# Kernel tuning notes

Hardware: AMD Instinct MI355X
Metric: run time of the kernel (lower is better)

The kernel has to match this reference:

```python
import math
import jax, jax.numpy as jnp
import numpy as np

N_EMBD = 1024
N_HEAD = 16
NUM_BUCKETS = 32
MAX_DISTANCE = 128


def _relative_position_bucket(relative_position, num_buckets=NUM_BUCKETS, max_distance=MAX_DISTANCE):
    # unidirectional (bidirectional=False): rp = -min(rp, 0)
    rp = -jnp.minimum(relative_position, 0)
    max_exact = num_buckets // 2
    is_small = rp < max_exact
    rp_large = max_exact + (
        jnp.log(rp.astype(jnp.float32) / max_exact + 1e-10)
        / math.log(max_distance / max_exact)
        * (num_buckets - max_exact)
    ).astype(jnp.int32)
    rp_large = jnp.minimum(rp_large, num_buckets - 1)
    return jnp.where(is_small, rp, rp_large)


def setup_inputs() -> dict:
    key = jax.random.key(0)
    ks = jax.random.split(key, 6)
    B, T, C = 4, 2048, N_EMBD
    s_in = 1.0 / math.sqrt(C)
    x = jax.random.normal(ks[0], (B, T, C), dtype=jnp.float32)
    W_attn = jax.random.normal(ks[1], (3 * C, C), dtype=jnp.float32) * s_in
    b_attn = jnp.zeros((3 * C,), dtype=jnp.float32)
    W_proj = jax.random.normal(ks[2], (C, C), dtype=jnp.float32) * s_in
    b_proj = jnp.zeros((C,), dtype=jnp.float32)
    rel_emb = jax.random.normal(ks[3], (NUM_BUCKETS, N_HEAD), dtype=jnp.float32) * 0.02
    return {"x": x, "W_attn": W_attn, "b_attn": b_attn,
            "W_proj": W_proj, "b_proj": b_proj, "rel_emb": rel_emb}


def reference(x, W_attn, b_attn, W_proj, b_proj, rel_emb):
    B, T, C = x.shape
    H = N_HEAD
    D = C // H
    qkv = x @ W_attn.T + b_attn              # [B,T,3C]
    q, k, v = jnp.split(qkv, 3, axis=-1)
    q = q.reshape(B, T, H, D).transpose(0, 2, 1, 3)  # [B,H,T,D]
    k = k.reshape(B, T, H, D).transpose(0, 2, 1, 3)
    v = v.reshape(B, T, H, D).transpose(0, 2, 1, 3)

    # T5 relative position bias (unidirectional)
    pos = jnp.arange(T)
    rel_pos = pos[None, :] - pos[:, None]            # [T,T] key - query
    buckets = _relative_position_bucket(rel_pos)     # [T,T]
    rel_bias = rel_emb[buckets]                      # [T,T,H]
    rel_bias = rel_bias.transpose(2, 0, 1)[None]     # [1,H,T,T]

    att = jnp.einsum('bhqd,bhkd->bhqk', q, k) * (1.0 / math.sqrt(D))
    att = att + rel_bias
    causal = jnp.tril(jnp.ones((T, T), dtype=bool))
    att = jnp.where(causal[None, None], att, -jnp.inf)
    att = jax.nn.softmax(att, axis=-1)
    y = jnp.einsum('bhqk,bhkd->bhqd', att, v)        # [B,H,T,D]
    y = y.transpose(0, 2, 1, 3).reshape(B, T, C)
    y = y @ W_proj.T + b_proj
    return y
```

## Files before the change

### kernel.cpp

```cpp
#include <hip/hip_runtime.h>
#include <hip/hip_bf16.h>

typedef __attribute__((ext_vector_type(8))) short short8;
typedef __attribute__((ext_vector_type(4))) short short4v;
typedef __attribute__((ext_vector_type(4))) float f32x4;

#define DEVI static __device__ __forceinline__

#define MTOK 8192
#define CDIM 1024
#define HN 16
#define HD 64
#define TSEQ 2048

#if defined(__has_builtin)
#if __has_builtin(__builtin_amdgcn_exp2f)
#define EXP2(x) __builtin_amdgcn_exp2f(x)
#else
#define EXP2(x) exp2f(x)
#endif
#else
#define EXP2(x) exp2f(x)
#endif

DEVI short bf16_rne(float f) {
  union { float f; unsigned u; } v; v.f = f;
  unsigned r = v.u + 0x7FFFu + ((v.u >> 16) & 1u);
  return (short)(r >> 16);
}

DEVI unsigned cvt_pk_bf16(float lo, float hi) {
  unsigned r;
  asm("v_cvt_pk_bf16_f32 %0, %1, %2" : "=v"(r) : "v"(lo), "v"(hi));
  return r;
}

DEVI void gload16(const void* g, void* l) {
  __builtin_amdgcn_global_load_lds(
      (const __attribute__((address_space(1))) void*)(unsigned long long)g,
      (__attribute__((address_space(3))) void*)(unsigned long long)l, 16, 0, 0);
}

#define MFMA_B16(A,B,C) __builtin_amdgcn_mfma_f32_16x16x32_bf16(A,B,C,0,0,0)

__global__ void pack_kernel(const float* __restrict__ x, const float* __restrict__ Wa,
                            const float* __restrict__ Wp,
                            short* __restrict__ xb, short* __restrict__ wab,
                            short* __restrict__ wpb) {
  const int NX4 = MTOK*CDIM/4, NA4 = 3*CDIM*CDIM/4, NP4 = CDIM*CDIM/4;
  const int total = NX4 + NA4 + NP4;
  for (int i = blockIdx.x*blockDim.x + threadIdx.x; i < total; i += gridDim.x*blockDim.x) {
    const float* src; short* dst; int off;
    if (i < NX4)          { src = x;  dst = xb;  off = i*4; }
    else if (i < NX4+NA4) { src = Wa; dst = wab; off = (i-NX4)*4; }
    else                  { src = Wp; dst = wpb; off = (i-NX4-NA4)*4; }
    float4 v = *(const float4*)(src + off);
    short4v r;
    r.x = bf16_rne(v.x); r.y = bf16_rne(v.y); r.z = bf16_rne(v.z); r.w = bf16_rne(v.w);
    *(short4v*)(dst + off) = r;
  }
}

__global__ void bias_table_kernel(const float* __restrict__ rel_emb, float* __restrict__ tab) {
  int d = blockIdx.x*blockDim.x + threadIdx.x;
  if (d >= TSEQ) return;
  int bucket;
  if (d < 16) bucket = d;
  else {
    int bl = 16 + (int)(logf((float)d / 16.0f + 1e-10f) / 2.0794415416798357f * 16.0f);
    bucket = bl < 31 ? bl : 31;
  }
  for (int h = 0; h < HN; h++) tab[h*TSEQ + d] = rel_emb[bucket*HN + h];
}

template<int EPI>
__global__ __launch_bounds__(512)
void gemm2(const short* __restrict__ A, const short* __restrict__ B,
           const float* __restrict__ bias,
           short* __restrict__ oq, short* __restrict__ ok, short* __restrict__ vt,
           float* __restrict__ of) {
  const int K = CDIM;
  int nbx = gridDim.x;
  int idx = blockIdx.y * nbx + blockIdx.x;
  int cpx = (nbx * gridDim.y) >> 3;
  int sw = (idx & 7) * cpx + (idx >> 3);
  int n0 = (sw % nbx) * 128, m0 = (sw / nbx) * 256;

  int tid = threadIdx.x, lane = tid & 63, w = tid >> 6;
  int wm = w >> 1, wn = w & 1;
  int r16 = lane & 15, g = lane >> 4;

  __shared__ __align__(16) short As[3][256*32];
  __shared__ __align__(16) short Bs[3][128*32];

  f32x4 zf = {0.f,0.f,0.f,0.f};
  f32x4 acc[4][4];
  #pragma unroll
  for (int mf = 0; mf < 4; mf++)
    #pragma unroll
    for (int nf = 0; nf < 4; nf++) acc[mf][nf] = zf;

  int r0 = tid >> 2;
  int cswz = (((tid & 3) ^ ((r0 >> 1) & 3)) << 3);
  long long aofs = (long long)(m0 + r0) * K + cswz;
  long long bofs = (long long)(n0 + r0) * K + cswz;

  auto STAGE = [&](int kt, int bi) {
    gload16(A + aofs + kt*32,          (short*)As[bi] + tid*8);
    gload16(A + aofs + kt*32 + 128*K,  (short*)As[bi] + 4096 + tid*8);
    gload16(B + bofs + kt*32,          (short*)Bs[bi] + tid*8);
  };

  STAGE(0, 0); STAGE(1, 1);
  asm volatile("s_waitcnt vmcnt(3)" ::: "memory");
  __builtin_amdgcn_s_barrier();
  __builtin_amdgcn_sched_barrier(0);

  int swz3 = (r16 >> 1) & 3;
  int fbA = (wm*64 + r16)*32 + ((g ^ swz3) << 3);
  int fbB = (wn*64 + r16)*32 + ((g ^ swz3) << 3);

  for (int kt = 0; kt < 32; kt++) {
    int cur = kt % 3;
    if (kt < 30) STAGE(kt + 2, (kt + 2) % 3);
    const short* Ab = As[cur];
    const short* Bb = Bs[cur];
    short8 af[4], bf[4];
    #pragma unroll
    for (int mf = 0; mf < 4; mf++) af[mf] = *(const short8*)(Ab + fbA + mf*512);
    #pragma unroll
    for (int nf = 0; nf < 4; nf++) bf[nf] = *(const short8*)(Bb + fbB + nf*512);
    __builtin_amdgcn_s_setprio(1);
    #pragma unroll
    for (int mf = 0; mf < 4; mf++)
      #pragma unroll
      for (int nf = 0; nf < 4; nf++)
        acc[mf][nf] = MFMA_B16(af[mf], bf[nf], acc[mf][nf]);
    __builtin_amdgcn_s_setprio(0);
    if (kt < 30) asm volatile("s_waitcnt vmcnt(3)" ::: "memory");
    else         asm volatile("s_waitcnt vmcnt(0)" ::: "memory");
    __builtin_amdgcn_s_barrier();
    __builtin_amdgcn_sched_barrier(0);
  }

  int b = m0 >> 11;
  int mrel = (m0 & 2047) + wm*64 + g*4;
  if constexpr (EPI == 0) {
    int which = n0 >> 10;
    int hh = ((n0 & 1023) >> 6) + wn;
    long long bh = (long long)(b*HN + hh);
    #pragma unroll
    for (int nf = 0; nf < 4; nf++) {
      int dd = nf*16 + r16;
      float bv = bias[n0 + wn*64 + dd];
      if (which == 2) {
        short* vdst = vt + (bh*HD + dd)*TSEQ + mrel;
        #pragma unroll
        for (int mf = 0; mf < 4; mf++) {
          short4v pv;
          #pragma unroll
          for (int j = 0; j < 4; j++) pv[j] = bf16_rne(acc[mf][nf][j] + bv);
          *(short4v*)(vdst + mf*16) = pv;
        }
      } else {
        short* odst = (which == 0 ? oq : ok) + bh*TSEQ*HD + dd;
        #pragma unroll
        for (int mf = 0; mf < 4; mf++)
          #pragma unroll
          for (int j = 0; j < 4; j++)
            odst[(long long)(mrel + mf*16 + j)*HD] = bf16_rne(acc[mf][nf][j] + bv);
      }
    }
  } else {
    #pragma unroll
    for (int nf = 0; nf < 4; nf++) {
      int col = n0 + wn*64 + nf*16 + r16;
      float bv = bias[col];
      #pragma unroll
      for (int mf = 0; mf < 4; mf++)
        #pragma unroll
        for (int j = 0; j < 4; j++)
          of[(long long)(m0 + wm*64 + mf*16 + g*4 + j)*CDIM + col] = acc[mf][nf][j] + bv;
    }
  }
}

__global__ __launch_bounds__(256)
void attn_kernel(const short* __restrict__ Qg, const short* __restrict__ Kg,
                 const short* __restrict__ Vtg, const float* __restrict__ btab,
                 short* __restrict__ outp) {
  int bh = blockIdx.x;
  int qb = 15 - (int)blockIdx.y;
  int h = bh & (HN-1), b = bh >> 4;
  int q0 = qb * 128;
  int tid = threadIdx.x, lane = tid & 63, w = tid >> 6;
  int r16 = lane & 15, g = lane >> 4;

  __shared__ __align__(16) short Ks[64*64];
  __shared__ __align__(16) short Vs[64*64];
  __shared__ __align__(16) short Ps[8][1024];
  __shared__ float bias_s[256];

  bias_s[tid & 255] = btab[h*TSEQ + (tid & 255)] * 1.44269504f;
  float cb = btab[h*TSEQ + 255] * 1.44269504f;

  short8 qa[2][2];
  #pragma unroll
  for (int mi = 0; mi < 2; mi++)
    #pragma unroll
    for (int ks = 0; ks < 2; ks++)
      qa[mi][ks] = *(const short8*)(Qg + ((long long)bh*TSEQ + q0 + w*32 + mi*16 + r16)*HD + ks*32 + g*8);

  f32x4 zf = {0.f,0.f,0.f,0.f};
  f32x4 o[2][4];
  #pragma unroll
  for (int mi = 0; mi < 2; mi++)
    #pragma unroll
    for (int c = 0; c < 4; c++) o[mi][c] = zf;
  float m_[2] = {-1e30f, -1e30f}, l_[2] = {0.f, 0.f};

  const short8 ones = {0x3f80,0x3f80,0x3f80,0x3f80,0x3f80,0x3f80,0x3f80,0x3f80};
  int qmax_wave = q0 + w*32 + 31;
  int swz = r16 & 7;
  int qrel = q0 + w*32 + r16;
  const float SC = 0.18033688f;

  for (int kb = 0; kb < q0 + 128; kb += 64) {
    #pragma unroll
    for (int i = 0; i < 2; i++) {
      int idx = tid + i*256;
      int r = idx >> 3;
      int cq = ((idx & 7) ^ (r & 7)) * 8;
      gload16(Kg  + ((long long)bh*TSEQ + kb + r)*HD + cq, (short*)Ks + idx*8);
      gload16(Vtg + ((long long)bh*HD  + r)*TSEQ + kb + cq, (short*)Vs + idx*8);
    }
    __syncthreads();
    if (kb <= qmax_wave) {
      f32x4 s[2][4];
      #pragma unroll
      for (int mi = 0; mi < 2; mi++)
        #pragma unroll
        for (int n = 0; n < 4; n++) s[mi][n] = zf;
      #pragma unroll
      for (int n = 0; n < 4; n++) {
        #pragma unroll
        for (int ks = 0; ks < 2; ks++) {
          short8 kf = *(const short8*)&Ks[(n*16 + r16)*64 + ((ks*4 + g) ^ swz)*8];
          s[0][n] = MFMA_B16(kf, qa[0][ks], s[0][n]);
          s[1][n] = MFMA_B16(kf, qa[1][ks], s[1][n]);
        }
      }
      bool far = (kb + 176 <= q0 + w*32);
      #pragma unroll
      for (int mi = 0; mi < 2; mi++) {
        char* prow = (char*)Ps[w*2 + mi] + r16*128 + ((g & 1) << 3);
        if (far) {
          float smax = s[mi][0][0];
          #pragma unroll
          for (int n = 0; n < 4; n++)
            #pragma unroll
            for (int j = 0; j < 4; j++) smax = fmaxf(smax, s[mi][n][j]);
          float mx = smax*SC + cb;
          mx = fmaxf(mx, __shfl_xor(mx, 16));
          mx = fmaxf(mx, __shfl_xor(mx, 32));
          float mnew;
          if (__all(mx <= m_[mi] + 8.0f)) {
            mnew = m_[mi];
          } else {
            mnew = fmaxf(m_[mi], mx);
            float corr = EXP2(m_[mi] - mnew);
            l_[mi] *= corr;
            #pragma unroll
            for (int c = 0; c < 4; c++) o[mi][c] *= corr;
            m_[mi] = mnew;
          }
          float cc = cb - mnew;
          #pragma unroll
          for (int n = 0; n < 4; n++) {
            unsigned u0 = cvt_pk_bf16(EXP2(__builtin_fmaf(s[mi][n][0], SC, cc)),
                                      EXP2(__builtin_fmaf(s[mi][n][1], SC, cc)));
            unsigned u1 = cvt_pk_bf16(EXP2(__builtin_fmaf(s[mi][n][2], SC, cc)),
                                      EXP2(__builtin_fmaf(s[mi][n][3], SC, cc)));
            *(uint2*)(prow + ((((n*2 + (g >> 1)) ^ swz)) << 4)) = make_uint2(u0, u1);
          }
        } else {
          int dbase = qrel + mi*16 - kb - g*4;
          float rowv[4][4];
          #pragma unroll
          for (int n = 0; n < 4; n++)
            #pragma unroll
            for (int j = 0; j < 4; j++) {
              int d = dbase - n*16 - j;
              rowv[n][j] = (d >= 0) ? s[mi][n][j]*SC + bias_s[d] : -1e30f;
            }
          float mx = rowv[0][0];
          #pragma unroll
          for (int n = 0; n < 4; n++)
            #pragma unroll
            for (int j = 0; j < 4; j++) mx = fmaxf(mx, rowv[n][j]);
          mx = fmaxf(mx, __shfl_xor(mx, 16));
          mx = fmaxf(mx, __shfl_xor(mx, 32));
          float mnew;
          if (__all(mx <= m_[mi] + 8.0f)) {
            mnew = m_[mi];
          } else {
            mnew = fmaxf(m_[mi], mx);
            float corr = EXP2(m_[mi] - mnew);
            l_[mi] *= corr;
            #pragma unroll
            for (int c = 0; c < 4; c++) o[mi][c] *= corr;
            m_[mi] = mnew;
          }
          #pragma unroll
          for (int n = 0; n < 4; n++) {
            unsigned u0 = cvt_pk_bf16(EXP2(rowv[n][0] - mnew), EXP2(rowv[n][1] - mnew));
            unsigned u1 = cvt_pk_bf16(EXP2(rowv[n][2] - mnew), EXP2(rowv[n][3] - mnew));
            *(uint2*)(prow + ((((n*2 + (g >> 1)) ^ swz)) << 4)) = make_uint2(u0, u1);
          }
        }
      }
      f32x4 lacc[2] = {zf, zf};
      #pragma unroll
      for (int ks = 0; ks < 2; ks++) {
        short8 pf0 = *(const short8*)((char*)Ps[w*2+0] + r16*128 + (((ks*4 + g) ^ swz) << 4));
        short8 pf1 = *(const short8*)((char*)Ps[w*2+1] + r16*128 + (((ks*4 + g) ^ swz) << 4));
        lacc[0] = MFMA_B16(ones, pf0, lacc[0]);
        lacc[1] = MFMA_B16(ones, pf1, lacc[1]);
        #pragma unroll
        for (int c = 0; c < 4; c++) {
          short8 vf = *(const short8*)&Vs[(c*16 + r16)*64 + ((ks*4 + g) ^ swz)*8];
          o[0][c] = MFMA_B16(vf, pf0, o[0][c]);
          o[1][c] = MFMA_B16(vf, pf1, o[1][c]);
        }
      }
      l_[0] += lacc[0][0];
      l_[1] += lacc[1][0];
    }
    __syncthreads();
  }

  #pragma unroll
  for (int mi = 0; mi < 2; mi++) {
    float inv = 1.0f / l_[mi];
    long long base = ((long long)(b*TSEQ + qrel + mi*16))*CDIM + h*HD;
    #pragma unroll
    for (int c = 0; c < 4; c++) {
      #pragma unroll
      for (int jj = 0; jj < 2; jj++) {
        unsigned pv = cvt_pk_bf16(o[mi][c][jj*2]*inv, o[mi][c][jj*2+1]*inv);
        *(unsigned*)(outp + base + c*16 + g*4 + jj*2) = pv;
      }
    }
  }
}

extern "C" void kernel_launch(void* const* d_in, const int* in_sizes, int n_in,
                              void* d_out, int out_size, void* d_ws, size_t ws_size,
                              hipStream_t stream) {
  (void)in_sizes; (void)n_in; (void)out_size; (void)ws_size;
  const float* x      = (const float*)d_in[0];
  const float* W_attn = (const float*)d_in[1];
  const float* b_attn = (const float*)d_in[2];
  const float* W_proj = (const float*)d_in[3];
  const float* b_proj = (const float*)d_in[4];
  const float* rel    = (const float*)d_in[5];
  float* out = (float*)d_out;
  char* ws = (char*)d_ws;

  short* xb   = (short*)(ws);
  short* wab  = (short*)(ws + 16777216LL);
  short* wpb  = (short*)(ws + 23068672LL);
  short* qbuf = (short*)(ws + 25165824LL);
  short* kbuf = (short*)(ws + 41943040LL);
  short* vt   = (short*)(ws + 58720256LL);
  short* att  = (short*)(ws + 75497472LL);
  float* tab  = (float*)(ws + 92274688LL);

  pack_kernel<<<2048, 256, 0, stream>>>(x, W_attn, W_proj, xb, wab, wpb);
  bias_table_kernel<<<8, 256, 0, stream>>>(rel, tab);
  gemm2<0><<<dim3(24, 32), 512, 0, stream>>>(xb, wab, b_attn, qbuf, kbuf, vt, nullptr);
  attn_kernel<<<dim3(64, 16), 256, 0, stream>>>(qbuf, kbuf, vt, tab, att);
  gemm2<1><<<dim3(8, 32), 512, 0, stream>>>(att, wpb, b_proj, nullptr, nullptr, nullptr, out);
}
```

Measured before the change: 249.7 us.

## Double-buffer K/V tiles in attention kernel with async global-to-LDS prefetch

Splits the K and V shared-memory tiles into two buffers and prefetches the tile two steps ahead, so global loads overlap the MFMA work on the current tile. The plain __syncthreads pairs are replaced by explicit vmcnt waits and raw barriers. This doubles K/V LDS use, which can lower occupancy. It also relies on the gload16 direct-to-LDS loads being counted by vmcnt, and if that counting assumption is wrong the results are incorrect.

Result: slower. 255.1 us (+2.2%).

```diff
diff --git a/kernel.cpp b/kernel.cpp
--- a/kernel.cpp
+++ b/kernel.cpp
@@ -196,13 +196,25 @@
   int tid = threadIdx.x, lane = tid & 63, w = tid >> 6;
   int r16 = lane & 15, g = lane >> 4;
 
-  __shared__ __align__(16) short Ks[64*64];
-  __shared__ __align__(16) short Vs[64*64];
+  __shared__ __align__(16) short Ks[2][64*64];
+  __shared__ __align__(16) short Vs[2][64*64];
   __shared__ __align__(16) short Ps[8][1024];
   __shared__ float bias_s[256];
 
   bias_s[tid & 255] = btab[h*TSEQ + (tid & 255)] * 1.44269504f;
   float cb = btab[h*TSEQ + 255] * 1.44269504f;
+
+  auto STAGE = [&](int t, int bi) {
+    int kb = t * 64;
+    #pragma unroll
+    for (int i = 0; i < 2; i++) {
+      int idx = tid + i*256;
+      int r = idx >> 3;
+      int cq = ((idx & 7) ^ (r & 7)) * 8;
+      gload16(Kg  + ((long long)bh*TSEQ + kb + r)*HD + cq, (short*)Ks[bi] + idx*8);
+      gload16(Vtg + ((long long)bh*HD  + r)*TSEQ + kb + cq, (short*)Vs[bi] + idx*8);
+    }
+  };
 
   short8 qa[2][2];
   #pragma unroll
@@ -224,17 +236,20 @@
   int swz = r16 & 7;
   int qrel = q0 + w*32 + r16;
   const float SC = 0.18033688f;
-
-  for (int kb = 0; kb < q0 + 128; kb += 64) {
-    #pragma unroll
-    for (int i = 0; i < 2; i++) {
-      int idx = tid + i*256;
-      int r = idx >> 3;
-      int cq = ((idx & 7) ^ (r & 7)) * 8;
-      gload16(Kg  + ((long long)bh*TSEQ + kb + r)*HD + cq, (short*)Ks + idx*8);
-      gload16(Vtg + ((long long)bh*HD  + r)*TSEQ + kb + cq, (short*)Vs + idx*8);
-    }
-    __syncthreads();
+  int ntiles = (q0 + 128) >> 6;
+
+  STAGE(0, 0);
+  STAGE(1, 1);
+  asm volatile("s_waitcnt lgkmcnt(0)" ::: "memory");
+
+  for (int t = 0; t < ntiles; t++) {
+    if (t + 1 < ntiles) asm volatile("s_waitcnt vmcnt(4)" ::: "memory");
+    else                asm volatile("s_waitcnt vmcnt(0)" ::: "memory");
+    __builtin_amdgcn_s_barrier();
+    __builtin_amdgcn_sched_barrier(0);
+    int kb = t * 64;
+    const short* Kb = Ks[t & 1];
+    const short* Vb = Vs[t & 1];
     if (kb <= qmax_wave) {
       f32x4 s[2][4];
       #pragma unroll
@@ -245,7 +260,7 @@
       for (int n = 0; n < 4; n++) {
         #pragma unroll
         for (int ks = 0; ks < 2; ks++) {
-          short8 kf = *(const short8*)&Ks[(n*16 + r16)*64 + ((ks*4 + g) ^ swz)*8];
+          short8 kf = *(const short8*)&Kb[(n*16 + r16)*64 + ((ks*4 + g) ^ swz)*8];
           s[0][n] = MFMA_B16(kf, qa[0][ks], s[0][n]);
           s[1][n] = MFMA_B16(kf, qa[1][ks], s[1][n]);
         }
@@ -328,7 +343,7 @@
         lacc[1] = MFMA_B16(ones, pf1, lacc[1]);
         #pragma unroll
         for (int c = 0; c < 4; c++) {
-          short8 vf = *(const short8*)&Vs[(c*16 + r16)*64 + ((ks*4 + g) ^ swz)*8];
+          short8 vf = *(const short8*)&Vb[(c*16 + r16)*64 + ((ks*4 + g) ^ swz)*8];
           o[0][c] = MFMA_B16(vf, pf0, o[0][c]);
           o[1][c] = MFMA_B16(vf, pf1, o[1][c]);
         }
@@ -336,7 +351,9 @@
       l_[0] += lacc[0][0];
       l_[1] += lacc[1][0];
     }
-    __syncthreads();
+    __builtin_amdgcn_s_barrier();
+    __builtin_amdgcn_sched_barrier(0);
+    if (t + 2 < ntiles) STAGE(t + 2, t & 1);
   }
 
   #pragma unroll
```
